# Performance work log

Measured on AMD Instinct MI355X. Metric: run time of the kernel, lower is better.

The kernel has to match this reference:

```python
import jax, jax.numpy as jnp
import numpy as np

B, L, NSTATE = 8192, 256, 9


def setup_inputs() -> dict:
    key = jax.random.key(0)
    k1, k2, k3, k4 = jax.random.split(key, 4)
    inputs = jax.random.normal(k1, (B, L, NSTATE), dtype=jnp.float32)
    path = jax.random.randint(k2, (B, L), 0, NSTATE, dtype=jnp.int32)
    # learned CRF params (init'd to zeros in the module; use small random for a
    # non-degenerate reference)
    tran = jax.random.normal(k3, (NSTATE, NSTATE), dtype=jnp.float32) * 0.1
    init = jax.random.normal(k4, (NSTATE,), dtype=jnp.float32) * 0.1
    return {"inputs": inputs, "path": path, "tran": tran, "init": init}


def reference(inputs, path, tran, init):
    # inputs: [B, L, S], path: [B, L], tran: [S, S], init: [S]
    # bio=False -> mask and imask are all zeros (no-op additions).
    # --- gold path score ---
    emit = jnp.take_along_axis(inputs, path[..., None], axis=-1)[..., 0]  # [B, L]
    tran_sc = tran[path[..., :-1], path[..., 1:]]                         # [B, L-1]
    path_scores = emit.sum(-1) + init[path[..., 0]] + tran_sc.sum(-1)     # [B]

    # --- partition function via log-semiring forward recurrence ---
    alpha0 = init + inputs[..., 0, :]                                     # [B, S]

    def step(alpha, x_t):
        # alpha: [B, S] (prev state), x_t: [B, S] (emission at t)
        nxt = alpha[..., :, None] + tran + x_t[..., None, :]              # [B, S, S]
        return jax.nn.logsumexp(nxt, axis=-2), None

    xs = jnp.moveaxis(inputs[..., 1:, :], -2, 0)                          # [L-1, B, S]
    alpha, _ = jax.lax.scan(step, alpha0, xs)
    scores = jax.nn.logsumexp(alpha, axis=-1)                             # [B]
    return scores - path_scores
```

## Files before the change

kernel.cpp:

```cpp
#include <hip/hip_runtime.h>


#define B_N 8192
#define L_N 256
#define SEQ_STRIDE 2304
#define HALF 128
#define SPB 6
#define XW 54
#define XSTRIDE 55
#define NBLK 22
#define PLS 129
#define SPW 16
#define NDIR_BLOCKS (B_N / SPW)

#define LOG2E 1.44269504088896340736f
#define LN2f  0.69314718055994530942f

#define QP1 57
#define QP2 78
#define QP3 147
#define QROT(src, CTRL) \
  __int_as_float(__builtin_amdgcn_mov_dpp(__float_as_int(src), CTRL, 0xf, 0xf, 0))

__device__ __forceinline__ void gl_lds4(const void* g, void* l) {
  __builtin_amdgcn_global_load_lds(
      (const __attribute__((address_space(1))) void*)g,
      (__attribute__((address_space(3))) void*)l, 4, 0, 0);
}

__device__ __forceinline__ float fexp(float x) {
  return __builtin_amdgcn_exp2f(x * LOG2E);
}

__global__ __launch_bounds__(64, 1) void crf_half(
    const float* __restrict__ xg, const int* __restrict__ path,
    const float* __restrict__ tran, const float* __restrict__ initv,
    float* __restrict__ ws)
{
  __shared__ float lx[2][SPW * XSTRIDE];
  __shared__ int   pl[SPW * PLS];
  __shared__ int   pl255[SPW];
  __shared__ float ltran[81];

  const int lane = threadIdx.x;
  const int c = lane & 3;
  const int q = lane >> 2;
  const bool fwd = (int)blockIdx.x < NDIR_BLOCKS;
  const int seq0 = (fwd ? blockIdx.x : blockIdx.x - NDIR_BLOCKS) * SPW;

  for (int i = lane; i < 81; i += 64) ltran[i] = tran[i];

  {
    const int t0 = fwd ? 0 : 127;
#pragma unroll
    for (int r = 0; r < SPW; ++r) {
      const int* g = path + (size_t)(seq0 + r) * L_N + t0 + lane;
      gl_lds4(g,      &pl[r * PLS]);
      gl_lds4(g + 64, &pl[r * PLS + 64]);
    }
  }
  if (!fwd && lane < SPW)
    pl255[lane] = path[(size_t)(seq0 + lane) * L_N + 255];

  if (lane < XW) {
    const int fb = fwd ? 0 : (SEQ_STRIDE - XW);
#pragma unroll
    for (int r = 0; r < SPW; ++r)
      gl_lds4(xg + (size_t)(seq0 + r) * SEQ_STRIDE + fb + lane,
              &lx[0][r * XSTRIDE]);
  }

  float Erot[4][3][3];
#pragma unroll
  for (int r = 0; r < 4; ++r)
#pragma unroll
    for (int k = 0; k < 3; ++k)
#pragma unroll
      for (int i = 0; i < 3; ++i) {
        const int ig = 3 * c + i;
        const int jg = 3 * ((c + r) & 3) + k;
        float v = 0.f;
        if (ig < 9 && jg < 9)
          v = fexp(fwd ? tran[jg * 9 + ig] : tran[ig * 9 + jg]);
        Erot[r][k][i] = v;
      }

  float o[3];
  float emit = 0.f, trn = 0.f;
  int ce = 0, pcur = 0;

  if (!fwd) {
#pragma unroll
    for (int k = 0; k < 3; ++k) o[k] = (c < 3) ? 1.f : 0.f;
    pcur = pl255[q];
  }

  const int myoff = (c == 3) ? 0 : 3 * c;

#pragma unroll 1
  for (int b = 0; b < NBLK; ++b) {
    asm volatile("s_waitcnt vmcnt(0)" ::: "memory");

    if (b + 1 < NBLK && lane < XW) {
      const int fb = fwd ? (b + 1) * XW : (SEQ_STRIDE - XW * (b + 2));
      float* dst = &lx[(b + 1) & 1][0];
#pragma unroll
      for (int r = 0; r < SPW; ++r)
        gl_lds4(xg + (size_t)(seq0 + r) * SEQ_STRIDE + fb + lane,
                dst + r * XSTRIDE);
    }

    const float* lxq = &lx[b & 1][q * XSTRIDE];

    float e[SPB * 3];
#pragma unroll
    for (int tt = 0; tt < SPB; ++tt)
#pragma unroll
      for (int k = 0; k < 3; ++k)
        e[tt * 3 + k] = fexp(lxq[tt * 9 + myoff + k]);

    if (fwd) {
#pragma unroll
      for (int kk = 0; kk < SPB; ++kk) {
        const int t = b * SPB + kk;
        if (t < HALF) {
          if (t == 0) {
#pragma unroll
            for (int k = 0; k < 3; ++k)
              o[k] = (c < 3) ? fexp(initv[3 * c + k] + lxq[myoff + k]) : 0.f;
            pcur = pl[q * PLS];
            emit = lxq[pcur];
          } else {
            float g[4][3];
#pragma unroll
            for (int k = 0; k < 3; ++k) {
              g[0][k] = o[k];
              g[1][k] = QROT(o[k], QP1);
              g[2][k] = QROT(o[k], QP2);
              g[3][k] = QROT(o[k], QP3);
            }
            if (kk == 0 && b > 0) {
              float m = g[0][0];
#pragma unroll
              for (int r = 0; r < 4; ++r)
#pragma unroll
                for (int k = 0; k < 3; ++k) m = fmaxf(m, g[r][k]);
              const int ex = (int)((__float_as_uint(m) >> 23) & 0xffu) - 126;
              ce += ex;
              const float sc = __uint_as_float((unsigned)(127 - ex) << 23);
#pragma unroll
              for (int r = 0; r < 4; ++r)
#pragma unroll
                for (int k = 0; k < 3; ++k) g[r][k] *= sc;
            }
            float out[3];
#pragma unroll
            for (int i = 0; i < 3; ++i) {
              float a = Erot[0][0][i] * g[0][0];
#pragma unroll
              for (int r = 0; r < 4; ++r)
#pragma unroll
                for (int k = 0; k < 3; ++k)
                  if (r + k > 0) a = fmaf(Erot[r][k][i], g[r][k], a);
              out[i] = a;
            }
            const int p = pl[q * PLS + t];
            emit += lxq[kk * 9 + p];
            trn  += ltran[pcur * 9 + p];
            pcur = p;
#pragma unroll
            for (int i = 0; i < 3; ++i) o[i] = out[i] * e[kk * 3 + i];
          }
        }
      }
    } else {
#pragma unroll
      for (int kk = 0; kk < SPB; ++kk) {
        const int t = 255 - b * SPB - kk;
        if (t >= HALF) {
          const int tt = SPB - 1 - kk;
          float w[3];
#pragma unroll
          for (int k = 0; k < 3; ++k) w[k] = e[tt * 3 + k] * o[k];
          float g[4][3];
#pragma unroll
          for (int k = 0; k < 3; ++k) {
            g[0][k] = w[k];
            g[1][k] = QROT(w[k], QP1);
            g[2][k] = QROT(w[k], QP2);
            g[3][k] = QROT(w[k], QP3);
          }
          if (kk == 0 && b > 0) {
            float m = g[0][0];
#pragma unroll
            for (int r = 0; r < 4; ++r)
#pragma unroll
              for (int k = 0; k < 3; ++k) m = fmaxf(m, g[r][k]);
            const int ex = (int)((__float_as_uint(m) >> 23) & 0xffu) - 126;
            ce += ex;
            const float sc = __uint_as_float((unsigned)(127 - ex) << 23);
#pragma unroll
            for (int r = 0; r < 4; ++r)
#pragma unroll
              for (int k = 0; k < 3; ++k) g[r][k] *= sc;
          }
#pragma unroll
          for (int i = 0; i < 3; ++i) {
            float a = Erot[0][0][i] * g[0][0];
#pragma unroll
            for (int r = 0; r < 4; ++r)
#pragma unroll
              for (int k = 0; k < 3; ++k)
                if (r + k > 0) a = fmaf(Erot[r][k][i], g[r][k], a);
            o[i] = a;
          }
          emit += lxq[tt * 9 + pcur];
          const int pm = pl[q * PLS + (t - 1 - 127)];
          trn += ltran[pm * 9 + pcur];
          pcur = pm;
        }
      }
    }
  }

  const int sq = seq0 + q;
  float* wp = ws + sq;
  if (fwd) {
    if (c < 3) {
#pragma unroll
      for (int k = 0; k < 3; ++k) wp[(3 * c + k) * B_N] = o[k];
    } else {
      wp[9 * B_N] = (float)ce;
      const int p0 = pl[q * PLS];
      wp[10 * B_N] = emit + trn + initv[p0];
    }
  } else {
    if (c < 3) {
#pragma unroll
      for (int k = 0; k < 3; ++k) wp[(11 + 3 * c + k) * B_N] = o[k];
    } else {
      wp[20 * B_N] = (float)ce;
      wp[21 * B_N] = emit + trn;
    }
  }
}

__global__ __launch_bounds__(256) void crf_combine(
    const float* __restrict__ ws, float* __restrict__ out)
{
  const int s = blockIdx.x * 256 + threadIdx.x;
  float dot = 0.f;
#pragma unroll
  for (int i = 0; i < 9; ++i)
    dot = fmaf(ws[i * B_N + s], ws[(11 + i) * B_N + s], dot);
  const float score =
      (__builtin_amdgcn_logf(dot) + ws[9 * B_N + s] + ws[20 * B_N + s]) * LN2f;
  out[s] = score - (ws[10 * B_N + s] + ws[21 * B_N + s]);
}

extern "C" void kernel_launch(void* const* d_in, const int* in_sizes, int n_in,
                              void* d_out, int out_size, void* d_ws, size_t ws_size,
                              hipStream_t stream) {
  (void)in_sizes; (void)n_in; (void)out_size; (void)ws_size;
  const float* xg    = (const float*)d_in[0];
  const int*   path  = (const int*)d_in[1];
  const float* tran  = (const float*)d_in[2];
  const float* initv = (const float*)d_in[3];
  float* ws  = (float*)d_ws;
  float* out = (float*)d_out;

  crf_half<<<2 * NDIR_BLOCKS, 64, 0, stream>>>(xg, path, tran, initv, ws);
  crf_combine<<<B_N / 256, 256, 0, stream>>>(ws, out);
}
```

Baseline: 133.7 us.

## Restructure CRF halves into 8-step windows with lane-split gold-path scoring

Each direction now processes 128 steps as 16 windows of 8 steps instead of 22 blocks of 6, which removes the t<HALF/t>=HALF guards and the wasted tail iterations. Gold-path emission and transition scoring is split across the 4 lanes of each quad (2 steps per lane) and reduced with DPP at the end, taking it off the serial per-step chain. Rescaling now runs after each window on the state vector with a cheap quad max, not on the rotated copies. The matvec uses two independent FMA chains to shorten dependency latency, and launch_bounds no longer pins one block per CU.

```diff
diff --git a/kernel.cpp b/kernel.cpp
--- a/kernel.cpp
+++ b/kernel.cpp
@@ -4,11 +4,10 @@
 #define B_N 8192
 #define L_N 256
 #define SEQ_STRIDE 2304
-#define HALF 128
-#define SPB 6
-#define XW 54
-#define XSTRIDE 55
-#define NBLK 22
+#define SPB 8
+#define XW 72
+#define XSTRIDE 73
+#define NW 16
 #define PLS 129
 #define SPW 16
 #define NDIR_BLOCKS (B_N / SPW)
@@ -32,14 +31,13 @@
   return __builtin_amdgcn_exp2f(x * LOG2E);
 }
 
-__global__ __launch_bounds__(64, 1) void crf_half(
+__global__ __launch_bounds__(64) void crf_half(
     const float* __restrict__ xg, const int* __restrict__ path,
     const float* __restrict__ tran, const float* __restrict__ initv,
     float* __restrict__ ws)
 {
   __shared__ float lx[2][SPW * XSTRIDE];
   __shared__ int   pl[SPW * PLS];
-  __shared__ int   pl255[SPW];
   __shared__ float ltran[81];
 
   const int lane = threadIdx.x;
@@ -53,22 +51,28 @@
   {
     const int t0 = fwd ? 0 : 127;
 #pragma unroll
-    for (int r = 0; r < SPW; ++r) {
-      const int* g = path + (size_t)(seq0 + r) * L_N + t0 + lane;
-      gl_lds4(g,      &pl[r * PLS]);
-      gl_lds4(g + 64, &pl[r * PLS + 64]);
+    for (int rr = 0; rr < SPW; ++rr) {
+      const int* g = path + (size_t)(seq0 + rr) * L_N + t0;
+      gl_lds4(g + lane, &pl[rr * PLS]);
+      gl_lds4(g + 64 + lane, &pl[rr * PLS + 64]);
     }
   }
   if (!fwd && lane < SPW)
-    pl255[lane] = path[(size_t)(seq0 + lane) * L_N + 255];
-
-  if (lane < XW) {
-    const int fb = fwd ? 0 : (SEQ_STRIDE - XW);
-#pragma unroll
-    for (int r = 0; r < SPW; ++r)
-      gl_lds4(xg + (size_t)(seq0 + r) * SEQ_STRIDE + fb + lane,
-              &lx[0][r * XSTRIDE]);
-  }
+    pl[lane * PLS + 128] = path[(size_t)(seq0 + lane) * L_N + 255];
+
+#define STAGE_X(FB, BI)                                                  \
+  { _Pragma("unroll")                                                    \
+    for (int rr = 0; rr < SPW; ++rr)                                     \
+      gl_lds4(xg + (size_t)(seq0 + rr) * SEQ_STRIDE + (FB) + lane,       \
+              &lx[(BI)][rr * XSTRIDE]);                                  \
+    if (lane < XW - 64) {                                                \
+      _Pragma("unroll")                                                  \
+      for (int rr = 0; rr < SPW; ++rr)                                   \
+        gl_lds4(xg + (size_t)(seq0 + rr) * SEQ_STRIDE + (FB) + 64 + lane,\
+                &lx[(BI)][rr * XSTRIDE + 64]);                           \
+    } }
+
+  if (fwd) { STAGE_X(0, 0) } else { STAGE_X(1152 + 72 * 15, 1) }
 
   float Erot[4][3][3];
 #pragma unroll
@@ -87,152 +91,138 @@
 
   float o[3];
   float emit = 0.f, trn = 0.f;
-  int ce = 0, pcur = 0;
-
+  int ce = 0;
   if (!fwd) {
 #pragma unroll
     for (int k = 0; k < 3; ++k) o[k] = (c < 3) ? 1.f : 0.f;
-    pcur = pl255[q];
   }
 
   const int myoff = (c == 3) ? 0 : 3 * c;
-
+  const int plq = q * PLS;
+
+#define MATVEC(IN)                                                       \
+  { float g1[3], g2[3], g3[3];                                           \
+    _Pragma("unroll")                                                    \
+    for (int k = 0; k < 3; ++k) {                                        \
+      g1[k] = QROT(IN[k], QP1);                                          \
+      g2[k] = QROT(IN[k], QP2);                                          \
+      g3[k] = QROT(IN[k], QP3);                                          \
+    }                                                                    \
+    _Pragma("unroll")                                                    \
+    for (int i = 0; i < 3; ++i) {                                        \
+      float aA = Erot[0][0][i] * IN[0];                                  \
+      aA = fmaf(Erot[0][1][i], IN[1], aA);                               \
+      aA = fmaf(Erot[0][2][i], IN[2], aA);                               \
+      aA = fmaf(Erot[1][0][i], g1[0], aA);                               \
+      aA = fmaf(Erot[1][1][i], g1[1], aA);                               \
+      aA = fmaf(Erot[1][2][i], g1[2], aA);                               \
+      float aB = Erot[2][0][i] * g2[0];                                  \
+      aB = fmaf(Erot[2][1][i], g2[1], aB);                               \
+      aB = fmaf(Erot[2][2][i], g2[2], aB);                               \
+      aB = fmaf(Erot[3][0][i], g3[0], aB);                               \
+      aB = fmaf(Erot[3][1][i], g3[1], aB);                               \
+      aB = fmaf(Erot[3][2][i], g3[2], aB);                               \
+      nxt[i] = aA + aB;                                                  \
+    } }
+
+#define RESCALE()                                                        \
+  { float m_ = fmaxf(fmaxf(o[0], o[1]), o[2]);                           \
+    m_ = fmaxf(m_, QROT(m_, QP1));                                       \
+    m_ = fmaxf(m_, QROT(m_, QP2));                                       \
+    const int ex_ = (int)((__float_as_uint(m_) >> 23) & 0xffu) - 126;    \
+    ce += ex_;                                                           \
+    const float sc_ = __uint_as_float((unsigned)(127 - ex_) << 23);      \
+    o[0] *= sc_; o[1] *= sc_; o[2] *= sc_; }
+
+  if (fwd) {
 #pragma unroll 1
-  for (int b = 0; b < NBLK; ++b) {
-    asm volatile("s_waitcnt vmcnt(0)" ::: "memory");
-
-    if (b + 1 < NBLK && lane < XW) {
-      const int fb = fwd ? (b + 1) * XW : (SEQ_STRIDE - XW * (b + 2));
-      float* dst = &lx[(b + 1) & 1][0];
-#pragma unroll
-      for (int r = 0; r < SPW; ++r)
-        gl_lds4(xg + (size_t)(seq0 + r) * SEQ_STRIDE + fb + lane,
-                dst + r * XSTRIDE);
-    }
-
-    const float* lxq = &lx[b & 1][q * XSTRIDE];
-
-    float e[SPB * 3];
-#pragma unroll
-    for (int tt = 0; tt < SPB; ++tt)
-#pragma unroll
-      for (int k = 0; k < 3; ++k)
-        e[tt * 3 + k] = fexp(lxq[tt * 9 + myoff + k]);
-
-    if (fwd) {
+    for (int w = 0; w < NW; ++w) {
+      asm volatile("s_waitcnt vmcnt(0)" ::: "memory");
+      if (w < NW - 1) { STAGE_X(72 * (w + 1), (w + 1) & 1) }
+      const float* lxq = &lx[w & 1][q * XSTRIDE];
+
+      {
+        const int s0 = 8 * w + 2 * c;
+        const int ps0 = pl[plq + s0];
+        const int ps1 = pl[plq + s0 + 1];
+        const int pp0 = pl[plq + (s0 > 0 ? s0 - 1 : 0)];
+        emit += lxq[(2 * c) * 9 + ps0] + lxq[(2 * c + 1) * 9 + ps1];
+        const float tv = ltran[pp0 * 9 + ps0];
+        trn += (s0 > 0 ? tv : 0.f) + ltran[ps0 * 9 + ps1];
+      }
+
+      float e[SPB * 3];
+#pragma unroll
+      for (int kk = 0; kk < SPB; ++kk)
+#pragma unroll
+        for (int k = 0; k < 3; ++k)
+          e[kk * 3 + k] = fexp(lxq[kk * 9 + myoff + k]);
+
 #pragma unroll
       for (int kk = 0; kk < SPB; ++kk) {
-        const int t = b * SPB + kk;
-        if (t < HALF) {
-          if (t == 0) {
-#pragma unroll
-            for (int k = 0; k < 3; ++k)
-              o[k] = (c < 3) ? fexp(initv[3 * c + k] + lxq[myoff + k]) : 0.f;
-            pcur = pl[q * PLS];
-            emit = lxq[pcur];
-          } else {
-            float g[4][3];
-#pragma unroll
-            for (int k = 0; k < 3; ++k) {
-              g[0][k] = o[k];
-              g[1][k] = QROT(o[k], QP1);
-              g[2][k] = QROT(o[k], QP2);
-              g[3][k] = QROT(o[k], QP3);
-            }
-            if (kk == 0 && b > 0) {
-              float m = g[0][0];
-#pragma unroll
-              for (int r = 0; r < 4; ++r)
-#pragma unroll
-                for (int k = 0; k < 3; ++k) m = fmaxf(m, g[r][k]);
-              const int ex = (int)((__float_as_uint(m) >> 23) & 0xffu) - 126;
-              ce += ex;
-              const float sc = __uint_as_float((unsigned)(127 - ex) << 23);
-#pragma unroll
-              for (int r = 0; r < 4; ++r)
-#pragma unroll
-                for (int k = 0; k < 3; ++k) g[r][k] *= sc;
-            }
-            float out[3];
-#pragma unroll
-            for (int i = 0; i < 3; ++i) {
-              float a = Erot[0][0][i] * g[0][0];
-#pragma unroll
-              for (int r = 0; r < 4; ++r)
-#pragma unroll
-                for (int k = 0; k < 3; ++k)
-                  if (r + k > 0) a = fmaf(Erot[r][k][i], g[r][k], a);
-              out[i] = a;
-            }
-            const int p = pl[q * PLS + t];
-            emit += lxq[kk * 9 + p];
-            trn  += ltran[pcur * 9 + p];
-            pcur = p;
-#pragma unroll
-            for (int i = 0; i < 3; ++i) o[i] = out[i] * e[kk * 3 + i];
-          }
+        if (w == 0 && kk == 0) {
+#pragma unroll
+          for (int k = 0; k < 3; ++k)
+            o[k] = (c < 3) ? fexp(initv[3 * c + k]) * e[k] : 0.f;
+        } else {
+          float nxt[3];
+          MATVEC(o)
+#pragma unroll
+          for (int i = 0; i < 3; ++i) o[i] = nxt[i] * e[kk * 3 + i];
         }
       }
-    } else {
-#pragma unroll
-      for (int kk = 0; kk < SPB; ++kk) {
-        const int t = 255 - b * SPB - kk;
-        if (t >= HALF) {
-          const int tt = SPB - 1 - kk;
-          float w[3];
-#pragma unroll
-          for (int k = 0; k < 3; ++k) w[k] = e[tt * 3 + k] * o[k];
-          float g[4][3];
-#pragma unroll
-          for (int k = 0; k < 3; ++k) {
-            g[0][k] = w[k];
-            g[1][k] = QROT(w[k], QP1);
-            g[2][k] = QROT(w[k], QP2);
-            g[3][k] = QROT(w[k], QP3);
-          }
-          if (kk == 0 && b > 0) {
-            float m = g[0][0];
-#pragma unroll
-            for (int r = 0; r < 4; ++r)
-#pragma unroll
-              for (int k = 0; k < 3; ++k) m = fmaxf(m, g[r][k]);
-            const int ex = (int)((__float_as_uint(m) >> 23) & 0xffu) - 126;
-            ce += ex;
-            const float sc = __uint_as_float((unsigned)(127 - ex) << 23);
-#pragma unroll
-            for (int r = 0; r < 4; ++r)
-#pragma unroll
-              for (int k = 0; k < 3; ++k) g[r][k] *= sc;
-          }
-#pragma unroll
-          for (int i = 0; i < 3; ++i) {
-            float a = Erot[0][0][i] * g[0][0];
-#pragma unroll
-            for (int r = 0; r < 4; ++r)
-#pragma unroll
-              for (int k = 0; k < 3; ++k)
-                if (r + k > 0) a = fmaf(Erot[r][k][i], g[r][k], a);
-            o[i] = a;
-          }
-          emit += lxq[tt * 9 + pcur];
-          const int pm = pl[q * PLS + (t - 1 - 127)];
-          trn += ltran[pm * 9 + pcur];
-          pcur = pm;
-        }
-      }
-    }
-  }
-
-  const int sq = seq0 + q;
-  float* wp = ws + sq;
+      RESCALE()
+    }
+  } else {
+#pragma unroll 1
+    for (int wi = 0; wi < NW; ++wi) {
+      const int w = NW - 1 - wi;
+      asm volatile("s_waitcnt vmcnt(0)" ::: "memory");
+      if (w > 0) { STAGE_X(1152 + 72 * (w - 1), (w - 1) & 1) }
+      const float* lxq = &lx[w & 1][q * XSTRIDE];
+
+      {
+        const int b0 = 8 * w + 2 * c;
+        const int ps0 = pl[plq + b0 + 1];
+        const int ps1 = pl[plq + b0 + 2];
+        const int pp0 = pl[plq + b0];
+        emit += lxq[(2 * c) * 9 + ps0] + lxq[(2 * c + 1) * 9 + ps1];
+        trn += ltran[pp0 * 9 + ps0] + ltran[ps0 * 9 + ps1];
+      }
+
+      float e[SPB * 3];
+#pragma unroll
+      for (int kk = 0; kk < SPB; ++kk)
+#pragma unroll
+        for (int k = 0; k < 3; ++k)
+          e[kk * 3 + k] = fexp(lxq[kk * 9 + myoff + k]);
+
+#pragma unroll
+      for (int kk = SPB - 1; kk >= 0; --kk) {
+        float wv[3];
+#pragma unroll
+        for (int k = 0; k < 3; ++k) wv[k] = e[kk * 3 + k] * o[k];
+        float nxt[3];
+        MATVEC(wv)
+#pragma unroll
+        for (int i = 0; i < 3; ++i) o[i] = nxt[i];
+      }
+      RESCALE()
+    }
+  }
+
+  float tot = emit + trn;
+  tot += QROT(tot, QP1);
+  tot += QROT(tot, QP2);
+
+  float* wp = ws + (seq0 + q);
   if (fwd) {
     if (c < 3) {
 #pragma unroll
       for (int k = 0; k < 3; ++k) wp[(3 * c + k) * B_N] = o[k];
     } else {
       wp[9 * B_N] = (float)ce;
-      const int p0 = pl[q * PLS];
-      wp[10 * B_N] = emit + trn + initv[p0];
+      wp[10 * B_N] = tot + initv[pl[plq]];
     }
   } else {
     if (c < 3) {
@@ -240,7 +230,7 @@
       for (int k = 0; k < 3; ++k) wp[(11 + 3 * c + k) * B_N] = o[k];
     } else {
       wp[20 * B_N] = (float)ce;
-      wp[21 * B_N] = emit + trn;
+      wp[21 * B_N] = tot;
     }
   }
 }
```

New measurement: 135.5 us. Within noise of the previous version (+1.3%).
